# Performance work log

Measured on AMD Instinct MI355X. Metric: run time of the kernel, lower is better.

The kernel has to match this reference:

```python
import jax, jax.numpy as jnp
import numpy as np

N = 131072   # total circuit nodes (tokens)
D = 128      # token_emb
E = 600000   # total ragged subgraph members (sum of len(pos)+len(pis) over gates)
G = 20000    # number of gates / subgraphs (len(g.gate))


def setup_inputs() -> dict:
    key = jax.random.key(0)
    ks = jax.random.split(key, 6)
    tf_hs = jax.random.normal(ks[0], (N, D), jnp.float32)
    tf_hf = jax.random.normal(ks[1], (N, D), jnp.float32)
    w_hs = jax.random.normal(ks[2], (D,), jnp.float32) / np.sqrt(D)
    w_hf = jax.random.normal(ks[3], (D,), jnp.float32) / np.sqrt(D)
    member_idx = jax.random.randint(ks[4], (E,), 0, N, dtype=jnp.int32)
    segment_ids = jnp.sort(jax.random.randint(ks[5], (E,), 0, G, dtype=jnp.int32))
    return {"tf_hs": tf_hs, "tf_hf": tf_hf, "w_hs": w_hs, "w_hf": w_hf,
            "member_idx": member_idx, "segment_ids": segment_ids}


def _attn_segment_pool(tok, member_idx, segment_ids, w):
    # Fused replacement for the per-gate python loop:
    #   hop[idx] = pool(cat([tok[pos_idx], tok[pis_idx]]))
    # tf_Pooling modeled as attention pooling: softmax(x @ w)-weighted sum per segment.
    x = tok[member_idx]                                  # [E, D] ragged gather
    logits = x @ w                                       # [E]
    m = jax.ops.segment_max(logits, segment_ids, num_segments=G)   # [G]
    m = jnp.where(jnp.isfinite(m), m, 0.0)               # guard empty segments
    p = jnp.exp(logits - m[segment_ids])                 # [E] stable softmax numerator
    z = jax.ops.segment_sum(p, segment_ids, num_segments=G)       # [G]
    attn = p / jnp.maximum(z, 1e-9)[segment_ids]         # [E]
    return jax.ops.segment_sum(attn[:, None] * x, segment_ids, num_segments=G)  # [G, D]


def reference(tf_hs, tf_hf, w_hs, w_hf, member_idx, segment_ids):
    hop_hs = _attn_segment_pool(tf_hs, member_idx, segment_ids, w_hs)
    hop_hf = _attn_segment_pool(tf_hf, member_idx, segment_ids, w_hf)
    return hop_hs, hop_hf
```

## Files before the change

### kernel.cpp

```cpp
#include <hip/hip_runtime.h>
#include <cmath>

#define D 128

typedef float __attribute__((ext_vector_type(4))) f32x4;

__device__ __forceinline__ uint pack_bf16_rne(float a, float b) {
    uint ua = __float_as_uint(a);
    uint ub = __float_as_uint(b);
    ua += 0x7fffu + ((ua >> 16) & 1u);
    ub += 0x7fffu + ((ub >> 16) & 1u);
    return (ua >> 16) | (ub & 0xffff0000u);
}

__device__ __forceinline__ float dot4(float4 x, float4 w) {
    return fmaf(x.x, w.x, fmaf(x.y, w.y, fmaf(x.z, w.z, x.w * w.w)));
}

__device__ __forceinline__ void do_pair(const f32x4* __restrict__ sh,
                                        const f32x4* __restrict__ sf,
                                        const float4* __restrict__ wh4,
                                        const float4* __restrict__ wf4,
                                        float* __restrict__ logit_hs,
                                        float* __restrict__ logit_hf,
                                        uint2* __restrict__ bhs,
                                        uint2* __restrict__ bhf,
                                        int row0, int lane, int N) {
    const int h = lane >> 5;
    const int c = lane & 31;
    const size_t base = (size_t)row0 * 32;
    const bool full = (row0 + 16 <= N);
    const float4 wh = wh4[c];
    const float4 wf = wf4[c];

    f32x4 xh[8], xf[8];
    #pragma unroll
    for (int k = 0; k < 8; ++k) {
        const int r = row0 + 2 * k + h;
        if (full || r < N) {
            xh[k] = __builtin_nontemporal_load(&sh[base + (size_t)k * 64 + lane]);
            xf[k] = __builtin_nontemporal_load(&sf[base + (size_t)k * 64 + lane]);
        } else {
            xh[k] = (f32x4)0.f;
            xf[k] = (f32x4)0.f;
        }
    }

    #pragma unroll
    for (int k = 0; k < 8; ++k) {
        const int r = row0 + 2 * k + h;
        if (full || r < N) {
            uint2 ph, pf;
            ph.x = pack_bf16_rne(xh[k].x, xh[k].y);
            ph.y = pack_bf16_rne(xh[k].z, xh[k].w);
            pf.x = pack_bf16_rne(xf[k].x, xf[k].y);
            pf.y = pack_bf16_rne(xf[k].z, xf[k].w);
            bhs[base + (size_t)k * 64 + lane] = ph;
            bhf[base + (size_t)k * 64 + lane] = pf;
        }
    }

    float ah[8], bh[8], af[8], bf[8];
    #pragma unroll
    for (int k = 0; k < 8; ++k) {
        float th = fmaf(xh[k].x, wh.x, fmaf(xh[k].y, wh.y,
                   fmaf(xh[k].z, wh.z, xh[k].w * wh.w)));
        float tf = fmaf(xf[k].x, wf.x, fmaf(xf[k].y, wf.y,
                   fmaf(xf[k].z, wf.z, xf[k].w * wf.w)));
        #pragma unroll
        for (int o = 1; o <= 16; o <<= 1) {
            th += __shfl_xor(th, o);
            tf += __shfl_xor(tf, o);
        }
        ah[k] = th; af[k] = tf;
        bh[k] = __shfl_xor(th, 32);
        bf[k] = __shfl_xor(tf, 32);
    }

    if (lane < 16 && row0 + lane < N) {
        const int k = lane >> 1;
        float vh0, vh1, vf0, vf1;
        switch (k) {
            case 0: vh0=ah[0]; vh1=bh[0]; vf0=af[0]; vf1=bf[0]; break;
            case 1: vh0=ah[1]; vh1=bh[1]; vf0=af[1]; vf1=bf[1]; break;
            case 2: vh0=ah[2]; vh1=bh[2]; vf0=af[2]; vf1=bf[2]; break;
            case 3: vh0=ah[3]; vh1=bh[3]; vf0=af[3]; vf1=bf[3]; break;
            case 4: vh0=ah[4]; vh1=bh[4]; vf0=af[4]; vf1=bf[4]; break;
            case 5: vh0=ah[5]; vh1=bh[5]; vf0=af[5]; vf1=bf[5]; break;
            case 6: vh0=ah[6]; vh1=bh[6]; vf0=af[6]; vf1=bf[6]; break;
            default: vh0=ah[7]; vh1=bh[7]; vf0=af[7]; vf1=bf[7]; break;
        }
        logit_hs[row0 + lane] = (lane & 1) ? vh1 : vh0;
        logit_hf[row0 + lane] = (lane & 1) ? vf1 : vf0;
    }
}

__global__ __launch_bounds__(256)
void prep_kernel(const float* __restrict__ tf_hs,
                 const float* __restrict__ tf_hf,
                 const float* __restrict__ w_hs,
                 const float* __restrict__ w_hf,
                 const int*   __restrict__ seg,
                 float* __restrict__ logit_hs,
                 float* __restrict__ logit_hf,
                 uint2* __restrict__ bhs,
                 uint2* __restrict__ bhf,
                 int*   __restrict__ starts,
                 int N, int E, int G, int RB) {
    if ((int)blockIdx.x >= RB) {
        const int e = (blockIdx.x - RB) * blockDim.x + threadIdx.x;
        if (e >= E) return;
        const int s = seg[e];
        if (e == 0) {
            for (int g = 0; g <= s; ++g) starts[g] = 0;
        } else {
            const int sp = seg[e - 1];
            for (int g = sp + 1; g <= s; ++g) starts[g] = e;
        }
        if (e == E - 1) {
            for (int g = s + 1; g <= G; ++g) starts[g] = E;
        }
        return;
    }

    const int lane = threadIdx.x & 63;
    const int wv   = threadIdx.x >> 6;
    const int row0 = blockIdx.x * 64 + wv * 16;
    if (row0 >= N) return;

    do_pair((const f32x4*)tf_hs, (const f32x4*)tf_hf,
            (const float4*)w_hs, (const float4*)w_hf,
            logit_hs, logit_hf, bhs, bhf, row0, lane, N);
}

__global__ __launch_bounds__(256, 4)
void pool_kernel_bf16(const uint2* __restrict__ bhs,
                      const uint2* __restrict__ bhf,
                      const float* __restrict__ logit_hs,
                      const float* __restrict__ logit_hf,
                      const int* __restrict__ member_idx,
                      const int* __restrict__ starts,
                      float* __restrict__ out, int G) {
    const int wid  = threadIdx.x >> 6;
    const int lane = threadIdx.x & 63;
    const int wgid = blockIdx.x * (blockDim.x >> 6) + wid;
    if (wgid >= 2 * G) return;
    const int pool = wgid >= G;
    const int gate = pool ? (wgid - G) : wgid;

    const uint2* tok    = pool ? bhf : bhs;
    const float* logit  = pool ? logit_hf : logit_hs;

    const int start = starts[gate];
    const int end   = starts[gate + 1];
    const int cnt   = end - start;

    const int half = lane >> 5;
    const int hl   = lane & 31;

    float4 acc = make_float4(0.f, 0.f, 0.f, 0.f);
    float m, iz;

    if (cnt <= 64) {
        const int  e   = start + lane;
        const bool v   = e < end;
        const int  row = v ? member_idx[e] : 0;
        const float l  = v ? logit[row] : -INFINITY;
        m = l;
        #pragma unroll
        for (int o = 32; o; o >>= 1) m = fmaxf(m, __shfl_xor(m, o));
        float p = v ? __expf(l - m) : 0.f;
        float z = p;
        #pragma unroll
        for (int o = 32; o; o >>= 1) z += __shfl_xor(z, o);
        iz = 1.f / fmaxf(z, 1e-9f);

        for (int j0 = 0; j0 < cnt; j0 += 32) {
            int rj[16]; float pj[16]; uint2 x[16];
            #pragma unroll
            for (int k = 0; k < 16; ++k) {
                const int src = j0 + 2 * k + half;
                rj[k] = __shfl(row, src);
                pj[k] = __shfl(p,   src);
            }
            #pragma unroll
            for (int k = 0; k < 16; ++k)
                x[k] = tok[(size_t)rj[k] * 32 + hl];
            #pragma unroll
            for (int k = 0; k < 16; ++k) {
                acc.x = fmaf(pj[k], __uint_as_float(x[k].x << 16),          acc.x);
                acc.y = fmaf(pj[k], __uint_as_float(x[k].x & 0xffff0000u),  acc.y);
                acc.z = fmaf(pj[k], __uint_as_float(x[k].y << 16),          acc.z);
                acc.w = fmaf(pj[k], __uint_as_float(x[k].y & 0xffff0000u),  acc.w);
            }
        }
    } else {
        m = -INFINITY; float z = 0.f;
        for (int e0 = start; e0 < end; e0 += 64) {
            const int  e   = e0 + lane;
            const bool v   = e < end;
            const int  row = v ? member_idx[e] : 0;
            const float l  = v ? logit[row] : -INFINITY;
            float cm = l;
            #pragma unroll
            for (int o = 32; o; o >>= 1) cm = fmaxf(cm, __shfl_xor(cm, o));
            const float nm = fmaxf(m, cm);
            z *= __expf(m - nm);
            m = nm;
            float pz = v ? __expf(l - m) : 0.f;
            #pragma unroll
            for (int o = 32; o; o >>= 1) pz += __shfl_xor(pz, o);
            z += pz;
        }
        iz = 1.f / fmaxf(z, 1e-9f);

        for (int e0 = start; e0 < end; e0 += 64) {
            const int  e   = e0 + lane;
            const bool v   = e < end;
            const int  row = v ? member_idx[e] : 0;
            const float l  = v ? logit[row] : -INFINITY;
            const float p  = v ? __expf(l - m) : 0.f;
            const int  jn  = min(64, end - e0);
            for (int j0 = 0; j0 < jn; j0 += 32) {
                int rj[16]; float pj[16]; uint2 x[16];
                #pragma unroll
                for (int k = 0; k < 16; ++k) {
                    const int src = j0 + 2 * k + half;
                    rj[k] = __shfl(row, src);
                    pj[k] = __shfl(p,   src);
                }
                #pragma unroll
                for (int k = 0; k < 16; ++k)
                    x[k] = tok[(size_t)rj[k] * 32 + hl];
                #pragma unroll
                for (int k = 0; k < 16; ++k) {
                    acc.x = fmaf(pj[k], __uint_as_float(x[k].x << 16),          acc.x);
                    acc.y = fmaf(pj[k], __uint_as_float(x[k].x & 0xffff0000u),  acc.y);
                    acc.z = fmaf(pj[k], __uint_as_float(x[k].y << 16),          acc.z);
                    acc.w = fmaf(pj[k], __uint_as_float(x[k].y & 0xffff0000u),  acc.w);
                }
            }
        }
    }

    acc.x += __shfl_xor(acc.x, 32);
    acc.y += __shfl_xor(acc.y, 32);
    acc.z += __shfl_xor(acc.z, 32);
    acc.w += __shfl_xor(acc.w, 32);
    if (half == 0) {
        float4* orow = (float4*)(out + ((size_t)pool * G + gate) * D);
        orow[hl] = make_float4(acc.x * iz, acc.y * iz, acc.z * iz, acc.w * iz);
    }
}

__global__ __launch_bounds__(256)
void logits_kernel_f32(const float* __restrict__ tf_hs,
                       const float* __restrict__ tf_hf,
                       const float* __restrict__ w_hs,
                       const float* __restrict__ w_hf,
                       const int*   __restrict__ seg,
                       float* __restrict__ logit_hs,
                       float* __restrict__ logit_hf,
                       int*   __restrict__ starts,
                       int N, int E, int G, int RB) {
    if ((int)blockIdx.x >= RB) {
        const int e = (blockIdx.x - RB) * blockDim.x + threadIdx.x;
        if (e >= E) return;
        const int s = seg[e];
        if (e == 0) { for (int g = 0; g <= s; ++g) starts[g] = 0; }
        else { const int sp = seg[e - 1]; for (int g = sp + 1; g <= s; ++g) starts[g] = e; }
        if (e == E - 1) { for (int g = s + 1; g <= G; ++g) starts[g] = E; }
        return;
    }
    const int lane = threadIdx.x & 63;
    const int wv   = threadIdx.x >> 6;
    const int row0 = blockIdx.x * 64 + wv * 16;
    if (row0 >= N) return;
    const int h = lane >> 5, c = lane & 31;
    const size_t base = (size_t)row0 * 32;
    const bool full = (row0 + 16 <= N);
    const float4* s4h = (const float4*)tf_hs;
    const float4* s4f = (const float4*)tf_hf;
    const float4 wlh = ((const float4*)w_hs)[c];
    const float4 wlf = ((const float4*)w_hf)[c];
    float a[8], bq[8];
    #pragma unroll
    for (int k = 0; k < 8; ++k) {
        const int r = row0 + 2 * k + h;
        const bool v = full || r < N;
        const float4 xh = v ? s4h[base + (size_t)k * 64 + lane] : make_float4(0,0,0,0);
        const float4 xf = v ? s4f[base + (size_t)k * 64 + lane] : make_float4(0,0,0,0);
        float ah = dot4(xh, wlh), af = dot4(xf, wlf);
        #pragma unroll
        for (int o = 1; o <= 16; o <<= 1) { ah += __shfl_xor(ah, o); af += __shfl_xor(af, o); }
        a[k] = ah; bq[k] = af;
    }
    float ao[8], bo[8];
    #pragma unroll
    for (int k = 0; k < 8; ++k) { ao[k] = __shfl_xor(a[k], 32); bo[k] = __shfl_xor(bq[k], 32); }
    if (lane < 16 && row0 + lane < N) {
        const int k = lane >> 1;
        float vh0, vh1, vf0, vf1;
        switch (k) {
            case 0: vh0=a[0]; vh1=ao[0]; vf0=bq[0]; vf1=bo[0]; break;
            case 1: vh0=a[1]; vh1=ao[1]; vf0=bq[1]; vf1=bo[1]; break;
            case 2: vh0=a[2]; vh1=ao[2]; vf0=bq[2]; vf1=bo[2]; break;
            case 3: vh0=a[3]; vh1=ao[3]; vf0=bq[3]; vf1=bo[3]; break;
            case 4: vh0=a[4]; vh1=ao[4]; vf0=bq[4]; vf1=bo[4]; break;
            case 5: vh0=a[5]; vh1=ao[5]; vf0=bq[5]; vf1=bo[5]; break;
            case 6: vh0=a[6]; vh1=ao[6]; vf0=bq[6]; vf1=bo[6]; break;
            default: vh0=a[7]; vh1=ao[7]; vf0=bq[7]; vf1=bo[7]; break;
        }
        logit_hs[row0 + lane] = (lane & 1) ? vh1 : vh0;
        logit_hf[row0 + lane] = (lane & 1) ? vf1 : vf0;
    }
}

__global__ __launch_bounds__(256, 4)
void pool_kernel_f32(const float* __restrict__ tf_hs,
                     const float* __restrict__ tf_hf,
                     const float* __restrict__ logit_hs,
                     const float* __restrict__ logit_hf,
                     const int* __restrict__ member_idx,
                     const int* __restrict__ starts,
                     float* __restrict__ out, int G) {
    const int wid  = threadIdx.x >> 6;
    const int lane = threadIdx.x & 63;
    const int wgid = blockIdx.x * (blockDim.x >> 6) + wid;
    if (wgid >= 2 * G) return;
    const int pool = wgid >= G;
    const int gate = pool ? (wgid - G) : wgid;

    const float2* tok   = (const float2*)(pool ? tf_hf : tf_hs);
    const float*  logit = pool ? logit_hf : logit_hs;

    const int start = starts[gate];
    const int end   = starts[gate + 1];

    float m = -INFINITY, z = 0.f;
    for (int e0 = start; e0 < end; e0 += 64) {
        const int  e   = e0 + lane;
        const bool v   = e < end;
        const int  row = v ? member_idx[e] : 0;
        const float l  = v ? logit[row] : -INFINITY;
        float cm = l;
        #pragma unroll
        for (int o = 32; o; o >>= 1) cm = fmaxf(cm, __shfl_xor(cm, o));
        const float nm = fmaxf(m, cm);
        z *= __expf(m - nm);
        m = nm;
        float pz = v ? __expf(l - m) : 0.f;
        #pragma unroll
        for (int o = 32; o; o >>= 1) pz += __shfl_xor(pz, o);
        z += pz;
    }
    const float izs = 1.f / fmaxf(z, 1e-9f);

    float2 acc = make_float2(0.f, 0.f);
    for (int e0 = start; e0 < end; e0 += 64) {
        const int  e   = e0 + lane;
        const bool v   = e < end;
        const int  row = v ? member_idx[e] : 0;
        const float l  = v ? logit[row] : -INFINITY;
        const float p  = v ? __expf(l - m) : 0.f;
        const int jn = min(64, end - e0);
        for (int j0 = 0; j0 < jn; j0 += 16) {
            int rj[16]; float pj[16]; float2 x[16];
            #pragma unroll
            for (int k = 0; k < 16; ++k) {
                rj[k] = __shfl(row, j0 + k);
                pj[k] = __shfl(p,   j0 + k);
            }
            #pragma unroll
            for (int k = 0; k < 16; ++k)
                x[k] = tok[(size_t)rj[k] * 64 + lane];
            #pragma unroll
            for (int k = 0; k < 16; ++k) {
                acc.x = fmaf(pj[k], x[k].x, acc.x);
                acc.y = fmaf(pj[k], x[k].y, acc.y);
            }
        }
    }
    float2* orow = (float2*)(out + ((size_t)pool * G + gate) * D);
    orow[lane] = make_float2(acc.x * izs, acc.y * izs);
}

extern "C" void kernel_launch(void* const* d_in, const int* in_sizes, int n_in,
                              void* d_out, int out_size, void* d_ws, size_t ws_size,
                              hipStream_t stream) {
    const float* tf_hs = (const float*)d_in[0];
    const float* tf_hf = (const float*)d_in[1];
    const float* w_hs  = (const float*)d_in[2];
    const float* w_hf  = (const float*)d_in[3];
    const int* member_idx  = (const int*)d_in[4];
    const int* segment_ids = (const int*)d_in[5];
    float* out = (float*)d_out;

    const int N = in_sizes[0] / D;
    const int E = in_sizes[4];
    const int G = out_size / (2 * D);

    const int RB = (N + 63) / 64;
    const int SB = (E + 255) / 256;
    const int nwaves = 2 * G;

    const size_t bf16_words = (size_t)N * 64;
    const size_t need = 2 * bf16_words * 4 + 2 * (size_t)N * 4 + (size_t)(G + 1) * 4;

    if (ws_size >= need) {
        uint*  bhs      = (uint*)d_ws;
        uint*  bhf      = bhs + bf16_words;
        float* logit_hs = (float*)(bhf + bf16_words);
        float* logit_hf = logit_hs + N;
        int*   starts   = (int*)(logit_hf + N);

        prep_kernel<<<RB + SB, 256, 0, stream>>>(
            tf_hs, tf_hf, w_hs, w_hf, segment_ids,
            logit_hs, logit_hf, (uint2*)bhs, (uint2*)bhf, starts,
            N, E, G, RB);
        pool_kernel_bf16<<<(nwaves + 3) / 4, 256, 0, stream>>>(
            (const uint2*)bhs, (const uint2*)bhf, logit_hs, logit_hf,
            member_idx, starts, out, G);
    } else {
        float* logit_hs = (float*)d_ws;
        float* logit_hf = logit_hs + N;
        int*   starts   = (int*)(logit_hf + N);

        logits_kernel_f32<<<RB + SB, 256, 0, stream>>>(
            tf_hs, tf_hf, w_hs, w_hf, segment_ids,
            logit_hs, logit_hf, starts, N, E, G, RB);
        pool_kernel_f32<<<(nwaves + 3) / 4, 256, 0, stream>>>(
            tf_hs, tf_hf, logit_hs, logit_hf, member_idx, starts, out, G);
    }
}
```

Measured before the change: 99.82 us.

## Stage member indices and weights in LDS, drop nontemporal loads, raise occupancy

In the pool kernel, each wave writes its (row, p) pairs to a shared-memory stage and reads them back as uint2. This replaces the 32 per-chunk shuffles used to broadcast member rows and softmax weights. The prep kernel switches from nontemporal f32x4 loads to plain float4 loads, split into separate hs and hf loops. Launch-bounds occupancy hints rise on both kernels (prep to 4, pool to 6). The LDS staging relies on intra-wave ordering with no barrier, and the tighter register budget may cause spills.

```diff
diff --git a/kernel.cpp b/kernel.cpp
--- a/kernel.cpp
+++ b/kernel.cpp
@@ -2,8 +2,6 @@
 #include <cmath>
 
 #define D 128
-
-typedef float __attribute__((ext_vector_type(4))) f32x4;
 
 __device__ __forceinline__ uint pack_bf16_rne(float a, float b) {
     uint ua = __float_as_uint(a);
@@ -17,8 +15,8 @@
     return fmaf(x.x, w.x, fmaf(x.y, w.y, fmaf(x.z, w.z, x.w * w.w)));
 }
 
-__device__ __forceinline__ void do_pair(const f32x4* __restrict__ sh,
-                                        const f32x4* __restrict__ sf,
+__device__ __forceinline__ void do_pair(const float4* __restrict__ sh,
+                                        const float4* __restrict__ sf,
                                         const float4* __restrict__ wh4,
                                         const float4* __restrict__ wf4,
                                         float* __restrict__ logit_hs,
@@ -33,29 +31,37 @@
     const float4 wh = wh4[c];
     const float4 wf = wf4[c];
 
-    f32x4 xh[8], xf[8];
+    float4 xh[8], xf[8];
+    #pragma unroll
+    for (int k = 0; k < 8; ++k) {
+        const int r = row0 + 2 * k + h;
+        const bool v = full || r < N;
+        xh[k] = v ? sh[base + (size_t)k * 64 + lane] : make_float4(0.f, 0.f, 0.f, 0.f);
+    }
+    #pragma unroll
+    for (int k = 0; k < 8; ++k) {
+        const int r = row0 + 2 * k + h;
+        const bool v = full || r < N;
+        xf[k] = v ? sf[base + (size_t)k * 64 + lane] : make_float4(0.f, 0.f, 0.f, 0.f);
+    }
+
     #pragma unroll
     for (int k = 0; k < 8; ++k) {
         const int r = row0 + 2 * k + h;
         if (full || r < N) {
-            xh[k] = __builtin_nontemporal_load(&sh[base + (size_t)k * 64 + lane]);
-            xf[k] = __builtin_nontemporal_load(&sf[base + (size_t)k * 64 + lane]);
-        } else {
-            xh[k] = (f32x4)0.f;
-            xf[k] = (f32x4)0.f;
-        }
-    }
-
+            uint2 ph;
+            ph.x = pack_bf16_rne(xh[k].x, xh[k].y);
+            ph.y = pack_bf16_rne(xh[k].z, xh[k].w);
+            bhs[base + (size_t)k * 64 + lane] = ph;
+        }
+    }
     #pragma unroll
     for (int k = 0; k < 8; ++k) {
         const int r = row0 + 2 * k + h;
         if (full || r < N) {
-            uint2 ph, pf;
-            ph.x = pack_bf16_rne(xh[k].x, xh[k].y);
-            ph.y = pack_bf16_rne(xh[k].z, xh[k].w);
+            uint2 pf;
             pf.x = pack_bf16_rne(xf[k].x, xf[k].y);
             pf.y = pack_bf16_rne(xf[k].z, xf[k].w);
-            bhs[base + (size_t)k * 64 + lane] = ph;
             bhf[base + (size_t)k * 64 + lane] = pf;
         }
     }
@@ -63,10 +69,8 @@
     float ah[8], bh[8], af[8], bf[8];
     #pragma unroll
     for (int k = 0; k < 8; ++k) {
-        float th = fmaf(xh[k].x, wh.x, fmaf(xh[k].y, wh.y,
-                   fmaf(xh[k].z, wh.z, xh[k].w * wh.w)));
-        float tf = fmaf(xf[k].x, wf.x, fmaf(xf[k].y, wf.y,
-                   fmaf(xf[k].z, wf.z, xf[k].w * wf.w)));
+        float th = dot4(xh[k], wh);
+        float tf = dot4(xf[k], wf);
         #pragma unroll
         for (int o = 1; o <= 16; o <<= 1) {
             th += __shfl_xor(th, o);
@@ -95,7 +99,7 @@
     }
 }
 
-__global__ __launch_bounds__(256)
+__global__ __launch_bounds__(256, 4)
 void prep_kernel(const float* __restrict__ tf_hs,
                  const float* __restrict__ tf_hf,
                  const float* __restrict__ w_hs,
@@ -128,12 +132,12 @@
     const int row0 = blockIdx.x * 64 + wv * 16;
     if (row0 >= N) return;
 
-    do_pair((const f32x4*)tf_hs, (const f32x4*)tf_hf,
+    do_pair((const float4*)tf_hs, (const float4*)tf_hf,
             (const float4*)w_hs, (const float4*)w_hf,
             logit_hs, logit_hf, bhs, bhf, row0, lane, N);
 }
 
-__global__ __launch_bounds__(256, 4)
+__global__ __launch_bounds__(256, 6)
 void pool_kernel_bf16(const uint2* __restrict__ bhs,
                       const uint2* __restrict__ bhf,
                       const float* __restrict__ logit_hs,
@@ -141,6 +145,8 @@
                       const int* __restrict__ member_idx,
                       const int* __restrict__ starts,
                       float* __restrict__ out, int G) {
+    __shared__ uint2 stage[4][64];
+
     const int wid  = threadIdx.x >> 6;
     const int lane = threadIdx.x & 63;
     const int wgid = blockIdx.x * (blockDim.x >> 6) + wid;
@@ -175,23 +181,23 @@
         for (int o = 32; o; o >>= 1) z += __shfl_xor(z, o);
         iz = 1.f / fmaxf(z, 1e-9f);
 
+        stage[wid][lane] = make_uint2((uint)row, __float_as_uint(p));
+
         for (int j0 = 0; j0 < cnt; j0 += 32) {
-            int rj[16]; float pj[16]; uint2 x[16];
+            uint2 mp[16]; uint2 x[16];
+            #pragma unroll
+            for (int k = 0; k < 16; ++k)
+                mp[k] = stage[wid][j0 + 2 * k + half];
+            #pragma unroll
+            for (int k = 0; k < 16; ++k)
+                x[k] = tok[(size_t)mp[k].x * 32 + hl];
             #pragma unroll
             for (int k = 0; k < 16; ++k) {
-                const int src = j0 + 2 * k + half;
-                rj[k] = __shfl(row, src);
-                pj[k] = __shfl(p,   src);
-            }
-            #pragma unroll
-            for (int k = 0; k < 16; ++k)
-                x[k] = tok[(size_t)rj[k] * 32 + hl];
-            #pragma unroll
-            for (int k = 0; k < 16; ++k) {
-                acc.x = fmaf(pj[k], __uint_as_float(x[k].x << 16),          acc.x);
-                acc.y = fmaf(pj[k], __uint_as_float(x[k].x & 0xffff0000u),  acc.y);
-                acc.z = fmaf(pj[k], __uint_as_float(x[k].y << 16),          acc.z);
-                acc.w = fmaf(pj[k], __uint_as_float(x[k].y & 0xffff0000u),  acc.w);
+                const float pk = __uint_as_float(mp[k].y);
+                acc.x = fmaf(pk, __uint_as_float(x[k].x << 16),          acc.x);
+                acc.y = fmaf(pk, __uint_as_float(x[k].x & 0xffff0000u),  acc.y);
+                acc.z = fmaf(pk, __uint_as_float(x[k].y << 16),          acc.z);
+                acc.w = fmaf(pk, __uint_as_float(x[k].y & 0xffff0000u),  acc.w);
             }
         }
     } else {
@@ -220,24 +226,23 @@
             const int  row = v ? member_idx[e] : 0;
             const float l  = v ? logit[row] : -INFINITY;
             const float p  = v ? __expf(l - m) : 0.f;
-            const int  jn  = min(64, end - e0);
+            stage[wid][lane] = make_uint2((uint)row, __float_as_uint(p));
+            const int jn = min(64, end - e0);
             for (int j0 = 0; j0 < jn; j0 += 32) {
-                int rj[16]; float pj[16]; uint2 x[16];
+                uint2 mp[16]; uint2 x[16];
+                #pragma unroll
+                for (int k = 0; k < 16; ++k)
+                    mp[k] = stage[wid][j0 + 2 * k + half];
+                #pragma unroll
+                for (int k = 0; k < 16; ++k)
+                    x[k] = tok[(size_t)mp[k].x * 32 + hl];
                 #pragma unroll
                 for (int k = 0; k < 16; ++k) {
-                    const int src = j0 + 2 * k + half;
-                    rj[k] = __shfl(row, src);
-                    pj[k] = __shfl(p,   src);
-                }
-                #pragma unroll
-                for (int k = 0; k < 16; ++k)
-                    x[k] = tok[(size_t)rj[k] * 32 + hl];
-                #pragma unroll
-                for (int k = 0; k < 16; ++k) {
-                    acc.x = fmaf(pj[k], __uint_as_float(x[k].x << 16),          acc.x);
-                    acc.y = fmaf(pj[k], __uint_as_float(x[k].x & 0xffff0000u),  acc.y);
-                    acc.z = fmaf(pj[k], __uint_as_float(x[k].y << 16),          acc.z);
-                    acc.w = fmaf(pj[k], __uint_as_float(x[k].y & 0xffff0000u),  acc.w);
+                    const float pk = __uint_as_float(mp[k].y);
+                    acc.x = fmaf(pk, __uint_as_float(x[k].x << 16),          acc.x);
+                    acc.y = fmaf(pk, __uint_as_float(x[k].x & 0xffff0000u),  acc.y);
+                    acc.z = fmaf(pk, __uint_as_float(x[k].y << 16),          acc.z);
+                    acc.w = fmaf(pk, __uint_as_float(x[k].y & 0xffff0000u),  acc.w);
                 }
             }
         }
```

After: 84.11 us. -15.7%, faster.
